# Kernel optimization log

Hardware: AMD Instinct MI355X
Metric: run time of the kernel (lower is better)

The kernel has to match this reference:

```python
import jax, jax.numpy as jnp
import numpy as np

CH = 256
B, H, W = 8, 64, 64


def _conv1x1(x, w, b):
    # x: [b, cin, h, w], w: [cout, cin], b: [cout]
    return jnp.einsum('bchw,oc->bohw', x, w) + b[None, :, None, None]


def setup_inputs() -> dict:
    key = jax.random.key(0)
    ks = jax.random.split(key, 6)
    s = 0.05  # weight scale (spectral-norm keeps weights O(1); scaled for stable softmax)
    return {
        'x': jax.random.normal(ks[0], (B, CH, H, W), dtype=jnp.float32),
        'wf': jax.random.normal(ks[1], (CH // 8, CH), dtype=jnp.float32) * s,
        'bf': jnp.zeros((CH // 8,), dtype=jnp.float32),
        'wg': jax.random.normal(ks[2], (CH // 8, CH), dtype=jnp.float32) * s,
        'bg': jnp.zeros((CH // 8,), dtype=jnp.float32),
        'wh': jax.random.normal(ks[3], (CH // 2, CH), dtype=jnp.float32) * s,
        'bh': jnp.zeros((CH // 2,), dtype=jnp.float32),
        'wv': jax.random.normal(ks[4], (CH, CH // 2), dtype=jnp.float32) * s,
        'bv': jnp.zeros((CH,), dtype=jnp.float32),
        'gamma': jnp.ones((1,), dtype=jnp.float32) * 0.5,
    }


def reference(x, wf, bf, wg, bg, wh, bh, wv, bv, gamma):
    b, c, h, w = x.shape
    n = h * w
    f = _conv1x1(x, wf, bf).reshape(b, -1, n)   # [b, c/8, n]
    g = _conv1x1(x, wg, bg).reshape(b, -1, n)   # [b, c/8, n]
    # scores = f^T g : [b, n, n]; softmax over last dim
    beta = jax.nn.softmax(jnp.einsum('bkn,bkm->bnm', f, g), axis=-1)
    h_ = _conv1x1(x, wh, bh).reshape(b, -1, n)  # [b, c/2, n]
    o = jnp.einsum('bcn,bnm->bcm', h_, beta).reshape(b, c // 2, h, w)
    o = _conv1x1(o, wv, bv)                      # [b, c, h, w]
    return x + gamma[0] * o
```

## Files before the change

### kernel.cpp

```cpp
#include <hip/hip_runtime.h>
#include <cstdint>

typedef float f32x4 __attribute__((ext_vector_type(4)));
typedef short bf16x8 __attribute__((ext_vector_type(8)));
typedef unsigned short u16x4 __attribute__((ext_vector_type(4)));
typedef unsigned uint4v __attribute__((ext_vector_type(4)));
typedef unsigned uint2v __attribute__((ext_vector_type(2)));

#define LOG2E 1.44269504088896340736f

#if __has_builtin(__builtin_amdgcn_exp2f)
#define EXP2(v) __builtin_amdgcn_exp2f(v)
#else
#define EXP2(v) exp2f(v)
#endif

#define GLD16(gp, lp) __builtin_amdgcn_global_load_lds( \
    (const __attribute__((address_space(1))) unsigned*)(const void*)(gp), \
    (__attribute__((address_space(3))) unsigned*)(void*)(lp), 16, 0, 0)

enum : unsigned {
    WALL_OFF  = 0u,
    BALL_OFF  = 98304u,
    WVF_OFF   = 99072u,
    FF_OFF    = 164608u,
    GF_OFF    = 2261760u,
    HF_OFF    = 4358912u,
    SCALE_OFF = 12747520u,
    ZPART_OFF = 12878592u,
    PART_OFF  = 13402880u,
};

static __device__ __forceinline__ unsigned short f2bf(float f) {
    unsigned u = __builtin_bit_cast(unsigned, f);
    u += 0x7fffu + ((u >> 16) & 1u);
    return (unsigned short)(u >> 16);
}

static __device__ __forceinline__ unsigned pk_bf(float lo, float hi) {
    unsigned a = __builtin_bit_cast(unsigned, hi) + 0x8000u;
    unsigned b = __builtin_bit_cast(unsigned, lo) + 0x8000u;
    return __builtin_amdgcn_perm(a, b, 0x07060302u);
}

static __device__ __forceinline__ f32x4 mfma_bf16(bf16x8 a, bf16x8 b, f32x4 c) {
    return __builtin_amdgcn_mfma_f32_16x16x32_bf16(a, b, c, 0, 0, 0);
}

__global__ __launch_bounds__(256) void k0_pack(const float* __restrict__ wf,
                                               const float* __restrict__ bfv,
                                               const float* __restrict__ wg,
                                               const float* __restrict__ bg,
                                               const float* __restrict__ wh,
                                               const float* __restrict__ bh,
                                               const float* __restrict__ wv,
                                               unsigned char* __restrict__ ws) {
    unsigned idx = blockIdx.x * 256u + threadIdx.x;
    unsigned short* Wall = (unsigned short*)(ws + WALL_OFF);
    float* ball = (float*)(ws + BALL_OFF);
    unsigned short* wvf = (unsigned short*)(ws + WVF_OFF);
    if (idx < 49152u) {
        unsigned k = idx >> 8;
        float v;
        if (k < 32u)      v = wf[idx] * LOG2E;
        else if (k < 64u) v = wg[idx - 8192u];
        else              v = wh[idx - 16384u];
        Wall[idx] = f2bf(v);
    } else if (idx < 49344u) {
        unsigned k = idx - 49152u;
        float v;
        if (k < 32u)      v = bfv[k] * LOG2E;
        else if (k < 64u) v = bg[k - 32u];
        else              v = bh[k - 64u];
        ball[k] = v;
    } else if (idx < 82112u) {
        unsigned jj = idx - 49344u;
        unsigned cc = jj >> 7, c = jj & 127u;
        unsigned cct = cc >> 4, lv = cc & 15u;
        unsigned ksv = c >> 5, qv = (c >> 3) & 3u, jv = c & 7u;
        wvf[(((cct * 4u + ksv) * 4u + qv) * 16u + lv) * 8u + jv] = f2bf(wv[jj]);
    }
}

__global__ __launch_bounds__(256) void k1_proj(const float* __restrict__ x,
                                               unsigned char* __restrict__ ws) {
    __shared__ unsigned XT[64 * 132];
    const int b = blockIdx.y;
    const int n0 = blockIdx.x * 64;
    const unsigned short* Wall = (const unsigned short*)(ws + WALL_OFF);
    const float* ball = (const float*)(ws + BALL_OFF);
    unsigned short* Ff = (unsigned short*)(ws + FF_OFF) + b * 131072;
    unsigned short* Gf = (unsigned short*)(ws + GF_OFF) + b * 131072;
    unsigned short* Hf = (unsigned short*)(ws + HF_OFF) + b * 524288;
    const int tid = threadIdx.x;
    const float* xb = x + b * (256 * 4096) + n0;
    {
        const int n4 = (tid & 15) * 4;
        const int crow = (tid >> 4) * 2;
        #pragma unroll
        for (int it = 0; it < 8; ++it) {
            const int c = crow + it * 32;
            const f32x4 r0 = *(const f32x4*)&xb[(size_t)c * 4096 + n4];
            const f32x4 r1 = *(const f32x4*)&xb[(size_t)(c + 1) * 4096 + n4];
            #pragma unroll
            for (int j = 0; j < 4; ++j)
                XT[(n4 + j) * 132 + (c >> 1)] = pk_bf(r0[j], r1[j]);
        }
    }
    __syncthreads();
    const int l = tid & 15, q = (tid >> 4) & 3, w = tid >> 6;
    const int nloc = w * 16 + l;
    const int ncol = n0 + nloc;
    bf16x8 bX[8];
    #pragma unroll
    for (int ks = 0; ks < 8; ++ks)
        bX[ks] = *(const bf16x8*)&XT[nloc * 132 + ks * 16 + q * 4];
    #pragma unroll
    for (int kt = 0; kt < 12; ++kt) {
        f32x4 acc = {0.f, 0.f, 0.f, 0.f};
        #pragma unroll
        for (int ks = 0; ks < 8; ++ks) {
            bf16x8 aW = *(const bf16x8*)&Wall[(kt * 16 + l) * 256 + ks * 32 + q * 8];
            acc = mfma_bf16(aW, bX[ks], acc);
        }
        const int kr0 = kt * 16 + q * 4;
        #pragma unroll
        for (int r = 0; r < 4; ++r) acc[r] += ball[kr0 + r];
        if (kt < 4) {
            const int kk = kt & 1;
            unsigned short* dst = (kt < 2) ? Ff : Gf;
            const int nt = ncol >> 4;
            const int qf = kk * 2 + (q >> 1), j0 = (q & 1) * 4;
            u16x4 pk;
            #pragma unroll
            for (int r = 0; r < 4; ++r) pk[r] = f2bf(acc[r]);
            *(u16x4*)&dst[(nt * 64 + qf * 16 + l) * 8 + j0] = pk;
        } else {
            const int ct = kt - 4;
            const int nt = ncol >> 5, qh = (ncol >> 3) & 3, jh = ncol & 7;
            #pragma unroll
            for (int r = 0; r < 4; ++r)
                Hf[((nt * 8 + ct) * 64 + qh * 16 + (q * 4 + r)) * 8 + jh] = f2bf(acc[r]);
        }
    }
}

__global__ __launch_bounds__(256) void k2_stats(unsigned char* __restrict__ ws) {
    const int b = blockIdx.y, zsl = blockIdx.z, tid = threadIdx.x;
    const int lane = tid & 63, l = tid & 15, q = (tid >> 4) & 3, w = tid >> 6;
    const unsigned short* Ff = (const unsigned short*)(ws + FF_OFF) + b * 131072;
    const unsigned short* Gf = (const unsigned short*)(ws + GF_OFF) + b * 131072;
    float* Zp = (float*)(ws + ZPART_OFF) + zsl * 32768 + b * 4096;
    const int n0 = blockIdx.x * 256 + w * 64;
    const int nt0 = n0 >> 4;
    bf16x8 aF[4];
    #pragma unroll
    for (int t = 0; t < 4; ++t)
        aF[t] = *(const bf16x8*)&Ff[((nt0 + t) * 64 + lane) * 8];
    f32x4 z[4];
    #pragma unroll
    for (int t = 0; t < 4; ++t) z[t] = (f32x4){0.f, 0.f, 0.f, 0.f};
    const int mt0 = zsl * 64;
    bf16x8 bG = *(const bf16x8*)&Gf[(mt0 * 64 + lane) * 8];
    for (int mt = 0; mt < 64; ++mt) {
        const bf16x8 g = bG;
        if (mt + 1 < 64)
            bG = *(const bf16x8*)&Gf[((mt0 + mt + 1) * 64 + lane) * 8];
        #pragma unroll
        for (int t = 0; t < 4; ++t) {
            f32x4 s = mfma_bf16(aF[t], g, (f32x4){0.f, 0.f, 0.f, 0.f});
            #pragma unroll
            for (int r = 0; r < 4; ++r)
                z[t][r] += EXP2(fminf(s[r], 100.f));
        }
    }
    #pragma unroll
    for (int off = 1; off < 16; off <<= 1)
        #pragma unroll
        for (int t = 0; t < 4; ++t)
            #pragma unroll
            for (int r = 0; r < 4; ++r)
                z[t][r] += __shfl_xor(z[t][r], off, 64);
    if (l == 0) {
        #pragma unroll
        for (int t = 0; t < 4; ++t)
            #pragma unroll
            for (int r = 0; r < 4; ++r)
                Zp[n0 + t * 16 + q * 4 + r] = z[t][r];
    }
}

__global__ __launch_bounds__(256) void k2b_inv(unsigned char* __restrict__ ws) {
    const float* zp = (const float*)(ws + ZPART_OFF);
    float* scale = (float*)(ws + SCALE_OFF);
    const int idx = (blockIdx.x * 256 + threadIdx.x) * 4;
    f32x4 s = *(const f32x4*)&zp[idx];
    s += *(const f32x4*)&zp[32768 + idx];
    s += *(const f32x4*)&zp[65536 + idx];
    s += *(const f32x4*)&zp[98304 + idx];
    f32x4 o;
    #pragma unroll
    for (int r = 0; r < 4; ++r) o[r] = 1.f / s[r];
    *(f32x4*)&scale[idx] = o;
}

__global__ __launch_bounds__(256, 2) void k3_attn(unsigned char* __restrict__ ws) {
    __shared__ __align__(16) unsigned short HT[2][4096];
    __shared__ __align__(16) unsigned short FTs[2][1024];
    __shared__ __align__(16) float SC[2048];
    const int tid = threadIdx.x;
    const int lane = tid & 63, l = tid & 15, q = (tid >> 4) & 3, w = tid >> 6;
    const int g = blockIdx.x & 15, bxm = blockIdx.x >> 4;
    const int b = g >> 1, nh = g & 1;
    const unsigned short* Ff = (const unsigned short*)(ws + FF_OFF) + b * 131072;
    const unsigned short* Gf = (const unsigned short*)(ws + GF_OFF) + b * 131072;
    const unsigned short* Hf = (const unsigned short*)(ws + HF_OFF) + b * 524288;
    const float* scale = (const float*)(ws + SCALE_OFF) + b * 4096 + nh * 2048;
    const int mt0 = bxm * 8 + w * 2;
    const bf16x8 bG0 = *(const bf16x8*)&Gf[(mt0 * 64 + lane) * 8];
    const bf16x8 bG1 = *(const bf16x8*)&Gf[((mt0 + 1) * 64 + lane) * 8];
    f32x4 acc0[8], acc1[8];
    #pragma unroll
    for (int ct = 0; ct < 8; ++ct) {
        acc0[ct] = (f32x4){0.f, 0.f, 0.f, 0.f};
        acc1[ct] = (f32x4){0.f, 0.f, 0.f, 0.f};
    }
    const bool qlo = q < 2;
    const int srcA = (q & 1) * 32 + l;
    const int srcB = srcA + 16;

    auto stage = [&](int i, int p) {
        const unsigned short* Hg = Hf + (size_t)(nh * 64 + i) * 4096;
        GLD16(Hg + ((w * 2 + 0) * 64 + lane) * 8, &HT[p][(w * 2 + 0) * 512]);
        GLD16(Hg + ((w * 2 + 1) * 64 + lane) * 8, &HT[p][(w * 2 + 1) * 512]);
        if (w < 2)
            GLD16(Ff + ((size_t)(nh * 128 + i * 2 + w) * 64 + lane) * 8, &FTs[p][w * 512]);
    };

    #pragma unroll
    for (int j = 0; j < 2; ++j)
        GLD16(scale + (w * 2 + j) * 256 + lane * 4, &SC[(w * 2 + j) * 256]);
    stage(0, 0);

    for (int i = 0; i < 64; ++i) {
        const int p = i & 1;
        __syncthreads();
        if (i + 1 < 64) stage(i + 1, p ^ 1);
        const bf16x8 aF0 = *(const bf16x8*)&FTs[p][lane * 8];
        const bf16x8 aF1 = *(const bf16x8*)&FTs[p][512 + lane * 8];
        const f32x4 c0 = *(const f32x4*)&SC[i * 32 + q * 4];
        const f32x4 c1 = *(const f32x4*)&SC[i * 32 + 16 + q * 4];
        const f32x4 zz = {0.f, 0.f, 0.f, 0.f};
        f32x4 s0 = mfma_bf16(aF0, bG0, zz);
        f32x4 s1 = mfma_bf16(aF1, bG0, zz);
        f32x4 s2 = mfma_bf16(aF0, bG1, zz);
        f32x4 s3 = mfma_bf16(aF1, bG1, zz);
        f32x4 e0, e1, e2, e3;
        #pragma unroll
        for (int r = 0; r < 4; ++r) {
            e0[r] = EXP2(fminf(s0[r], 100.f)) * c0[r];
            e1[r] = EXP2(fminf(s1[r], 100.f)) * c1[r];
            e2[r] = EXP2(fminf(s2[r], 100.f)) * c0[r];
            e3[r] = EXP2(fminf(s3[r], 100.f)) * c1[r];
        }
        const unsigned a01 = pk_bf(e0[0], e0[1]), a23 = pk_bf(e0[2], e0[3]);
        const unsigned b01 = pk_bf(e1[0], e1[1]), b23 = pk_bf(e1[2], e1[3]);
        const unsigned g01 = pk_bf(e2[0], e2[1]), g23 = pk_bf(e2[2], e2[3]);
        const unsigned h01 = pk_bf(e3[0], e3[1]), h23 = pk_bf(e3[2], e3[3]);
        uint4v r0, r1;
        {
            int tA, tB;
            tA = __shfl((int)a01, srcA, 64); tB = __shfl((int)b01, srcA, 64);
            r0[0] = (unsigned)(qlo ? tA : tB);
            tA = __shfl((int)a23, srcA, 64); tB = __shfl((int)b23, srcA, 64);
            r0[1] = (unsigned)(qlo ? tA : tB);
            tA = __shfl((int)a01, srcB, 64); tB = __shfl((int)b01, srcB, 64);
            r0[2] = (unsigned)(qlo ? tA : tB);
            tA = __shfl((int)a23, srcB, 64); tB = __shfl((int)b23, srcB, 64);
            r0[3] = (unsigned)(qlo ? tA : tB);
            tA = __shfl((int)g01, srcA, 64); tB = __shfl((int)h01, srcA, 64);
            r1[0] = (unsigned)(qlo ? tA : tB);
            tA = __shfl((int)g23, srcA, 64); tB = __shfl((int)h23, srcA, 64);
            r1[1] = (unsigned)(qlo ? tA : tB);
            tA = __shfl((int)g01, srcB, 64); tB = __shfl((int)h01, srcB, 64);
            r1[2] = (unsigned)(qlo ? tA : tB);
            tA = __shfl((int)g23, srcB, 64); tB = __shfl((int)h23, srcB, 64);
            r1[3] = (unsigned)(qlo ? tA : tB);
        }
        const bf16x8 bE0 = __builtin_bit_cast(bf16x8, r0);
        const bf16x8 bE1 = __builtin_bit_cast(bf16x8, r1);
        #pragma unroll
        for (int ct = 0; ct < 8; ++ct) {
            const bf16x8 aH = *(const bf16x8*)&HT[p][ct * 512 + lane * 8];
            acc0[ct] = mfma_bf16(aH, bE0, acc0[ct]);
            acc1[ct] = mfma_bf16(aH, bE1, acc1[ct]);
        }
    }
    unsigned short* P = (unsigned short*)(ws + PART_OFF);
    const size_t mb = (size_t)(b * 2 + nh) * 4096 + bxm * 128;
    #pragma unroll
    for (int ct = 0; ct < 8; ++ct) {
        uint2v p0, p1;
        p0[0] = pk_bf(acc0[ct][0], acc0[ct][1]);
        p0[1] = pk_bf(acc0[ct][2], acc0[ct][3]);
        p1[0] = pk_bf(acc1[ct][0], acc1[ct][1]);
        p1[1] = pk_bf(acc1[ct][2], acc1[ct][3]);
        *(uint2v*)&P[(mb + w * 32 + l) * 128 + ct * 16 + q * 4] = p0;
        *(uint2v*)&P[(mb + w * 32 + 16 + l) * 128 + ct * 16 + q * 4] = p1;
    }
}

__global__ __launch_bounds__(256) void k4_out(const float* __restrict__ x,
                                              const float* __restrict__ bv,
                                              const float* __restrict__ gamma,
                                              float* __restrict__ out,
                                              unsigned char* __restrict__ ws) {
    const int b = blockIdx.y, tid = threadIdx.x;
    const int lane = tid & 63, l = tid & 15, q = (tid >> 4) & 3, w = tid >> 6;
    const unsigned short* P = (const unsigned short*)(ws + PART_OFF);
    const unsigned short* Wvf = (const unsigned short*)(ws + WVF_OFF);
    const int mg = blockIdx.x * 64 + w * 16 + l;
    const size_t b0 = ((size_t)(b * 2 + 0) * 4096 + mg) * 128;
    const size_t b1 = ((size_t)(b * 2 + 1) * 4096 + mg) * 128;
    bf16x8 bO[4];
    #pragma unroll
    for (int ks = 0; ks < 4; ++ks) {
        const uint4v u0 = *(const uint4v*)&P[b0 + ks * 32 + q * 8];
        const uint4v u1 = *(const uint4v*)&P[b1 + ks * 32 + q * 8];
        uint4v s;
        #pragma unroll
        for (int j = 0; j < 4; ++j) {
            const float alo = __builtin_bit_cast(float, u0[j] << 16);
            const float ahi = __builtin_bit_cast(float, u0[j] & 0xffff0000u);
            const float blo = __builtin_bit_cast(float, u1[j] << 16);
            const float bhi = __builtin_bit_cast(float, u1[j] & 0xffff0000u);
            s[j] = pk_bf(alo + blo, ahi + bhi);
        }
        bO[ks] = __builtin_bit_cast(bf16x8, s);
    }
    const float gam = gamma[0];
    const float* xb = x + b * (256 * 4096);
    float* ob = out + b * (256 * 4096);
    #pragma unroll
    for (int cct = 0; cct < 16; ++cct) {
        f32x4 f = {0.f, 0.f, 0.f, 0.f};
        #pragma unroll
        for (int ks = 0; ks < 4; ++ks) {
            const bf16x8 aV = *(const bf16x8*)&Wvf[((cct * 4 + ks) * 64 + lane) * 8];
            f = mfma_bf16(aV, bO[ks], f);
        }
        #pragma unroll
        for (int r = 0; r < 4; ++r) {
            const int cc = cct * 16 + q * 4 + r;
            ob[cc * 4096 + mg] = xb[cc * 4096 + mg] + gam * (f[r] + bv[cc]);
        }
    }
}

extern "C" void kernel_launch(void* const* d_in, const int* in_sizes, int n_in,
                              void* d_out, int out_size, void* d_ws, size_t ws_size,
                              hipStream_t stream) {
    const float* x   = (const float*)d_in[0];
    const float* wf  = (const float*)d_in[1];
    const float* bfv = (const float*)d_in[2];
    const float* wg  = (const float*)d_in[3];
    const float* bg  = (const float*)d_in[4];
    const float* wh  = (const float*)d_in[5];
    const float* bh  = (const float*)d_in[6];
    const float* wv  = (const float*)d_in[7];
    const float* bv  = (const float*)d_in[8];
    const float* gam = (const float*)d_in[9];
    float* out = (float*)d_out;
    unsigned char* ws = (unsigned char*)d_ws;
    (void)in_sizes; (void)n_in; (void)out_size; (void)ws_size;

    hipLaunchKernelGGL(k0_pack, dim3(321), dim3(256), 0, stream,
                       wf, bfv, wg, bg, wh, bh, wv, ws);
    hipLaunchKernelGGL(k1_proj, dim3(64, 8), dim3(256), 0, stream, x, ws);
    hipLaunchKernelGGL(k2_stats, dim3(16, 8, 4), dim3(256), 0, stream, ws);
    hipLaunchKernelGGL(k2b_inv, dim3(32), dim3(256), 0, stream, ws);
    hipLaunchKernelGGL(k3_attn, dim3(512), dim3(256), 0, stream, ws);
    hipLaunchKernelGGL(k4_out, dim3(64, 8), dim3(256), 0, stream,
                       x, bv, gam, out, ws);
}
```

Before: 238.0 us.

## Fold softmax normalizer into MFMA accumulator and split attention four ways

```diff
diff --git a/kernel.cpp b/kernel.cpp
--- a/kernel.cpp
+++ b/kernel.cpp
@@ -13,6 +13,11 @@
 #define EXP2(v) __builtin_amdgcn_exp2f(v)
 #else
 #define EXP2(v) exp2f(v)
+#endif
+#if __has_builtin(__builtin_amdgcn_logf)
+#define LOG2F(v) __builtin_amdgcn_logf(v)
+#else
+#define LOG2F(v) __log2f(v)
 #endif
 
 #define GLD16(gp, lp) __builtin_amdgcn_global_load_lds( \
@@ -171,7 +176,7 @@
             f32x4 s = mfma_bf16(aF[t], g, (f32x4){0.f, 0.f, 0.f, 0.f});
             #pragma unroll
             for (int r = 0; r < 4; ++r)
-                z[t][r] += EXP2(fminf(s[r], 100.f));
+                z[t][r] += EXP2(s[r]);
         }
     }
     #pragma unroll
@@ -200,22 +205,26 @@
     s += *(const f32x4*)&zp[98304 + idx];
     f32x4 o;
     #pragma unroll
-    for (int r = 0; r < 4; ++r) o[r] = 1.f / s[r];
+    for (int r = 0; r < 4; ++r) o[r] = -LOG2F(s[r]);
     *(f32x4*)&scale[idx] = o;
 }
 
-__global__ __launch_bounds__(256, 2) void k3_attn(unsigned char* __restrict__ ws) {
+template<int NS>
+__global__ __launch_bounds__(256, NS) void k3_attn(unsigned char* __restrict__ ws) {
+    constexpr int NITER = 128 / NS;
+    constexpr int NGRP = 8 * NS;
+    constexpr int NQ = 4096 / NS;
     __shared__ __align__(16) unsigned short HT[2][4096];
     __shared__ __align__(16) unsigned short FTs[2][1024];
-    __shared__ __align__(16) float SC[2048];
+    __shared__ __align__(16) float SC[NQ];
     const int tid = threadIdx.x;
     const int lane = tid & 63, l = tid & 15, q = (tid >> 4) & 3, w = tid >> 6;
-    const int g = blockIdx.x & 15, bxm = blockIdx.x >> 4;
-    const int b = g >> 1, nh = g & 1;
+    const int g = blockIdx.x % NGRP, bxm = blockIdx.x / NGRP;
+    const int b = g / NS, nh = g % NS;
     const unsigned short* Ff = (const unsigned short*)(ws + FF_OFF) + b * 131072;
     const unsigned short* Gf = (const unsigned short*)(ws + GF_OFF) + b * 131072;
     const unsigned short* Hf = (const unsigned short*)(ws + HF_OFF) + b * 524288;
-    const float* scale = (const float*)(ws + SCALE_OFF) + b * 4096 + nh * 2048;
+    const float* lsc = (const float*)(ws + SCALE_OFF) + b * 4096 + nh * NQ;
     const int mt0 = bxm * 8 + w * 2;
     const bf16x8 bG0 = *(const bf16x8*)&Gf[(mt0 * 64 + lane) * 8];
     const bf16x8 bG1 = *(const bf16x8*)&Gf[((mt0 + 1) * 64 + lane) * 8];
@@ -230,38 +239,41 @@
     const int srcB = srcA + 16;
 
     auto stage = [&](int i, int p) {
-        const unsigned short* Hg = Hf + (size_t)(nh * 64 + i) * 4096;
+        const unsigned short* Hg = Hf + (size_t)(nh * NITER + i) * 4096;
         GLD16(Hg + ((w * 2 + 0) * 64 + lane) * 8, &HT[p][(w * 2 + 0) * 512]);
         GLD16(Hg + ((w * 2 + 1) * 64 + lane) * 8, &HT[p][(w * 2 + 1) * 512]);
         if (w < 2)
-            GLD16(Ff + ((size_t)(nh * 128 + i * 2 + w) * 64 + lane) * 8, &FTs[p][w * 512]);
+            GLD16(Ff + ((size_t)((nh * NITER + i) * 2 + w) * 64 + lane) * 8,
+                  &FTs[p][w * 512]);
     };
 
-    #pragma unroll
-    for (int j = 0; j < 2; ++j)
-        GLD16(scale + (w * 2 + j) * 256 + lane * 4, &SC[(w * 2 + j) * 256]);
+    {
+        constexpr int CH = NQ / 256;
+        #pragma unroll
+        for (int j = w; j < CH; j += 4)
+            GLD16(lsc + j * 256 + lane * 4, &SC[j * 256]);
+    }
     stage(0, 0);
 
-    for (int i = 0; i < 64; ++i) {
+    for (int i = 0; i < NITER; ++i) {
         const int p = i & 1;
         __syncthreads();
-        if (i + 1 < 64) stage(i + 1, p ^ 1);
+        if (i + 1 < NITER) stage(i + 1, p ^ 1);
         const bf16x8 aF0 = *(const bf16x8*)&FTs[p][lane * 8];
         const bf16x8 aF1 = *(const bf16x8*)&FTs[p][512 + lane * 8];
         const f32x4 c0 = *(const f32x4*)&SC[i * 32 + q * 4];
         const f32x4 c1 = *(const f32x4*)&SC[i * 32 + 16 + q * 4];
-        const f32x4 zz = {0.f, 0.f, 0.f, 0.f};
-        f32x4 s0 = mfma_bf16(aF0, bG0, zz);
-        f32x4 s1 = mfma_bf16(aF1, bG0, zz);
-        f32x4 s2 = mfma_bf16(aF0, bG1, zz);
-        f32x4 s3 = mfma_bf16(aF1, bG1, zz);
+        f32x4 s0 = mfma_bf16(aF0, bG0, c0);
+        f32x4 s1 = mfma_bf16(aF1, bG0, c1);
+        f32x4 s2 = mfma_bf16(aF0, bG1, c0);
+        f32x4 s3 = mfma_bf16(aF1, bG1, c1);
         f32x4 e0, e1, e2, e3;
         #pragma unroll
         for (int r = 0; r < 4; ++r) {
-            e0[r] = EXP2(fminf(s0[r], 100.f)) * c0[r];
-            e1[r] = EXP2(fminf(s1[r], 100.f)) * c1[r];
-            e2[r] = EXP2(fminf(s2[r], 100.f)) * c0[r];
-            e3[r] = EXP2(fminf(s3[r], 100.f)) * c1[r];
+            e0[r] = EXP2(s0[r]);
+            e1[r] = EXP2(s1[r]);
+            e2[r] = EXP2(s2[r]);
+            e3[r] = EXP2(s3[r]);
         }
         const unsigned a01 = pk_bf(e0[0], e0[1]), a23 = pk_bf(e0[2], e0[3]);
         const unsigned b01 = pk_bf(e1[0], e1[1]), b23 = pk_bf(e1[2], e1[3]);
@@ -297,7 +309,7 @@
         }
     }
     unsigned short* P = (unsigned short*)(ws + PART_OFF);
-    const size_t mb = (size_t)(b * 2 + nh) * 4096 + bxm * 128;
+    const size_t mb = (size_t)(b * NS + nh) * 4096 + bxm * 128;
     #pragma unroll
     for (int ct = 0; ct < 8; ++ct) {
         uint2v p0, p1;
@@ -310,6 +322,7 @@
     }
 }
 
+template<int NS>
 __global__ __launch_bounds__(256) void k4_out(const float* __restrict__ x,
                                               const float* __restrict__ bv,
                                               const float* __restrict__ gamma,
@@ -320,22 +333,23 @@
     const unsigned short* P = (const unsigned short*)(ws + PART_OFF);
     const unsigned short* Wvf = (const unsigned short*)(ws + WVF_OFF);
     const int mg = blockIdx.x * 64 + w * 16 + l;
-    const size_t b0 = ((size_t)(b * 2 + 0) * 4096 + mg) * 128;
-    const size_t b1 = ((size_t)(b * 2 + 1) * 4096 + mg) * 128;
     bf16x8 bO[4];
     #pragma unroll
     for (int ks = 0; ks < 4; ++ks) {
-        const uint4v u0 = *(const uint4v*)&P[b0 + ks * 32 + q * 8];
-        const uint4v u1 = *(const uint4v*)&P[b1 + ks * 32 + q * 8];
+        float lo[4] = {0.f, 0.f, 0.f, 0.f}, hi[4] = {0.f, 0.f, 0.f, 0.f};
+        #pragma unroll
+        for (int h = 0; h < NS; ++h) {
+            const size_t bh = ((size_t)(b * NS + h) * 4096 + mg) * 128;
+            const uint4v u = *(const uint4v*)&P[bh + ks * 32 + q * 8];
+            #pragma unroll
+            for (int j = 0; j < 4; ++j) {
+                lo[j] += __builtin_bit_cast(float, u[j] << 16);
+                hi[j] += __builtin_bit_cast(float, u[j] & 0xffff0000u);
+            }
+        }
         uint4v s;
         #pragma unroll
-        for (int j = 0; j < 4; ++j) {
-            const float alo = __builtin_bit_cast(float, u0[j] << 16);
-            const float ahi = __builtin_bit_cast(float, u0[j] & 0xffff0000u);
-            const float blo = __builtin_bit_cast(float, u1[j] << 16);
-            const float bhi = __builtin_bit_cast(float, u1[j] & 0xffff0000u);
-            s[j] = pk_bf(alo + blo, ahi + bhi);
-        }
+        for (int j = 0; j < 4; ++j) s[j] = pk_bf(lo[j], hi[j]);
         bO[ks] = __builtin_bit_cast(bf16x8, s);
     }
     const float gam = gamma[0];
@@ -372,14 +386,24 @@
     const float* gam = (const float*)d_in[9];
     float* out = (float*)d_out;
     unsigned char* ws = (unsigned char*)d_ws;
-    (void)in_sizes; (void)n_in; (void)out_size; (void)ws_size;
+    (void)in_sizes; (void)n_in; (void)out_size;
 
     hipLaunchKernelGGL(k0_pack, dim3(321), dim3(256), 0, stream,
                        wf, bfv, wg, bg, wh, bh, wv, ws);
     hipLaunchKernelGGL(k1_proj, dim3(64, 8), dim3(256), 0, stream, x, ws);
     hipLaunchKernelGGL(k2_stats, dim3(16, 8, 4), dim3(256), 0, stream, ws);
     hipLaunchKernelGGL(k2b_inv, dim3(32), dim3(256), 0, stream, ws);
-    hipLaunchKernelGGL(k3_attn, dim3(512), dim3(256), 0, stream, ws);
-    hipLaunchKernelGGL(k4_out, dim3(64, 8), dim3(256), 0, stream,
-                       x, bv, gam, out, ws);
-}
+
+    const size_t need4 = (size_t)PART_OFF + (size_t)8 * 4 * 4096 * 128 * 2;
+    if (ws_size >= need4) {
+        hipLaunchKernelGGL(HIP_KERNEL_NAME(k3_attn<4>), dim3(1024), dim3(256),
+                           0, stream, ws);
+        hipLaunchKernelGGL(HIP_KERNEL_NAME(k4_out<4>), dim3(64, 8), dim3(256),
+                           0, stream, x, bv, gam, out, ws);
+    } else {
+        hipLaunchKernelGGL(HIP_KERNEL_NAME(k3_attn<2>), dim3(512), dim3(256),
+                           0, stream, ws);
+        hipLaunchKernelGGL(HIP_KERNEL_NAME(k4_out<2>), dim3(64, 8), dim3(256),
+                           0, stream, x, bv, gam, out, ws);
+    }
+}
```

Result: faster. 219.1 us (-7.9%).
